# Performance work log

Hardware: AMD Instinct MI355X
Metric: run time of the kernel (lower is better)

Reference implementation:

```python
import jax, jax.numpy as jnp
import numpy as np

BETA, THR, ALPHA = 0.9, 1.0, 2.0  # snn.Leaky defaults from neuron_options + surrogate.atan(alpha=2)

# Heaviside spike with atan surrogate gradient (snntorch surrogate.atan)
@jax.custom_vjp
def spike(u):
    return (u > 0).astype(u.dtype)

def _spk_fwd(u):
    return (u > 0).astype(u.dtype), u

def _spk_bwd(u, g):
    return ((ALPHA / 2) / (1 + (jnp.pi / 2 * ALPHA * u) ** 2) * g,)

spike.defvjp(_spk_fwd, _spk_bwd)


def setup_inputs() -> dict:
    key = jax.random.key(0)
    ks = jax.random.split(key, 4)
    B, T, I, H1, H2, O = 128, 128, 1024, 2048, 2048, 512
    return {
        "x": jax.random.normal(ks[0], (B, T, I), jnp.float32),
        "W1": jax.random.normal(ks[1], (H1, I), jnp.float32) * 0.02,
        "b1": jnp.zeros((H1,), jnp.float32),
        "W2": jax.random.normal(ks[2], (H2, H1), jnp.float32) * 0.02,
        "b2": jnp.zeros((H2,), jnp.float32),
        "Wout": jax.random.normal(ks[3], (O, H2), jnp.float32) * 0.02,
        "bout": jnp.zeros((O,), jnp.float32),
    }


def _lif(v_prev, cur):
    # Module calls snn.Leaky as spike_layer(in_volt, x) -> forward(input_=v_prev, mem=cur).
    # snntorch Leaky ('subtract' reset): reset = H(mem - thr) [detached];
    # mem_new = beta*mem + input_ - reset*thr; spk = H(mem_new - thr) with atan surrogate.
    reset = jax.lax.stop_gradient((cur > THR).astype(cur.dtype))
    mem = BETA * cur + v_prev - reset * THR
    return spike(mem - THR), mem


def reference(x, W1, b1, W2, b2, Wout, bout):
    B, T, I = x.shape
    H1, H2 = W1.shape[0], W2.shape[0]
    v0 = (jnp.zeros((B, H1), x.dtype), jnp.zeros((B, H2), x.dtype))

    def step(vs, x_t):
        v1, v2 = vs
        s1, v1n = _lif(v1, x_t @ W1.T + b1)   # linear -> LIF layer 1
        s2, v2n = _lif(v2, s1 @ W2.T + b2)    # linear -> LIF layer 2
        return (v1n, v2n), s2

    _, spikes = jax.lax.scan(step, v0, jnp.swapaxes(x, 0, 1))  # spikes: (T, B, H2)
    acc = spikes.mean(0)  # 'sum' accumulator = mean over time of last-layer spikes
    return acc @ Wout.T + bout  # fc_out, identity activation
```

## Files before the change

### kernel.cpp

```cpp
#include <hip/hip_runtime.h>


typedef unsigned long long u64;
typedef __attribute__((ext_vector_type(4))) float f32x4;
typedef __attribute__((ext_vector_type(8))) short bf16x8;

__device__ __forceinline__ unsigned short f2bf(float f) {
  unsigned u = __float_as_uint(f);
  u += 0x7fff + ((u >> 16) & 1);
  return (unsigned short)(u >> 16);
}
__device__ __forceinline__ float bf2f(unsigned short h) {
  return __uint_as_float(((unsigned)h) << 16);
}
__device__ __forceinline__ void gld_lds16(const unsigned short* g, unsigned short* l) {
  __builtin_amdgcn_global_load_lds((const __attribute__((address_space(1))) void*)g,
                                   (__attribute__((address_space(3))) void*)l, 16, 0, 0);
}

__global__ void k_split4(const float4* __restrict__ src, unsigned short* __restrict__ dst,
                         int lgK, size_t total4) {
  size_t i = (size_t)blockIdx.x * 256 + threadIdx.x;
  if (i >= total4) return;
  const int K = 1 << lgK;
  size_t e = i << 2;
  size_t r = e >> lgK;
  int k = (int)(e & (size_t)(K - 1));
  float4 f = src[i];
  unsigned short h0 = f2bf(f.x), h1 = f2bf(f.y), h2 = f2bf(f.z), h3 = f2bf(f.w);
  unsigned short l0 = f2bf(f.x - bf2f(h0)), l1 = f2bf(f.y - bf2f(h1));
  unsigned short l2 = f2bf(f.z - bf2f(h2)), l3 = f2bf(f.w - bf2f(h3));
  size_t o = (r << (lgK + 1)) + (size_t)k;
  *(u64*)(dst + o)     = (u64)h0 | ((u64)h1 << 16) | ((u64)h2 << 32) | ((u64)h3 << 48);
  *(u64*)(dst + o + K) = (u64)l0 | ((u64)l1 << 16) | ((u64)l2 << 32) | ((u64)l3 << 48);
}

#define DSR4(D, BASE)                                                          \
  do {                                                                         \
    asm volatile("ds_read_b128 %0, %1" : "=v"(D[0]) : "v"(BASE));              \
    asm volatile("ds_read_b128 %0, %1 offset:2048" : "=v"(D[1]) : "v"(BASE));  \
    asm volatile("ds_read_b128 %0, %1 offset:4096" : "=v"(D[2]) : "v"(BASE));  \
    asm volatile("ds_read_b128 %0, %1 offset:6144" : "=v"(D[3]) : "v"(BASE));  \
  } while (0)
#define WAITL(N)                                                               \
  do {                                                                         \
    asm volatile("s_waitcnt lgkmcnt(" #N ")" ::: "memory");                    \
    __builtin_amdgcn_sched_barrier(0);                                         \
  } while (0)
#define VM0() asm volatile("s_waitcnt vmcnt(0)" ::: "memory")
#define BAR() __builtin_amdgcn_s_barrier()
#define MFMA16(MH, AF, BG)                                                     \
  _Pragma("unroll")                                                            \
  for (int m = 0; m < 4; ++m)                                                  \
    _Pragma("unroll")                                                          \
    for (int n = 0; n < 4; ++n)                                                \
      acc[(MH)*4 + m][n] = __builtin_amdgcn_mfma_f32_16x16x32_bf16(            \
          AF[m], BG[n], acc[(MH)*4 + m][n], 0, 0, 0);

template <int LAYER>
__global__ __launch_bounds__(512, 2)
void k_gemm_lif(const unsigned short* __restrict__ A,
                const unsigned short* __restrict__ Bw,
                const float* __restrict__ bias,
                unsigned short* __restrict__ out, int b0) {
  __shared__ __align__(128) char lds[132096];
  const int NKT = (LAYER == 1) ? 48 : 32;
  const int ldB = (LAYER == 1) ? 2048 : 4096;
  const int tid  = threadIdx.x;
  const int lane = tid & 63;
  const int w    = tid >> 6;
  const int wm = w >> 2, wn = w & 3;
  const int wr = wm * 128, wc = wn * 64;
  const int lrow = lane & 15, t4 = lane >> 4;
  const int brow = blockIdx.x * 256, bcol = blockIdx.y * 256;

  f32x4 acc[8][4];
#pragma unroll
  for (int m = 0; m < 8; ++m)
#pragma unroll
    for (int n = 0; n < 4; ++n) acc[m][n] = (f32x4){0.f, 0.f, 0.f, 0.f};

  int voffA[4], voffB[4];
  unsigned dstA[4], dstB[4];
#pragma unroll
  for (int j = 0; j < 4; ++j) {
    const int c = tid + j * 512;
    const int r = c >> 3;
    const int scol = ((c & 7) ^ (r & 7)) * 8;
    voffA[j] = (brow + r) * 2048 + scol;
    voffB[j] = (bcol + r) * ldB + scol;
    dstA[j] = (unsigned)c * 16;
    dstB[j] = 32768u + (unsigned)c * 16;
  }

  auto stage_tile = [&](int tt) {
    if (tt >= NKT) return;
    const int kb = tt * 64;
    int aoff, boff;
    if (LAYER == 1) {
      aoff = (kb < 1024) ? kb : kb - 1024;
      boff = (kb < 2048) ? kb : kb - 2048;
    } else {
      aoff = kb;
      boff = kb;
    }
    const unsigned short* Ap = A + aoff;
    const unsigned short* Bp = Bw + boff;
    char* slot = lds + (tt & 1) * 65536;
#pragma unroll
    for (int j = 0; j < 4; ++j)
      gld_lds16(Ap + voffA[j], (unsigned short*)(slot + dstA[j]));
#pragma unroll
    for (int j = 0; j < 4; ++j)
      gld_lds16(Bp + voffB[j], (unsigned short*)(slot + dstB[j]));
  };

  const unsigned ldsb = (unsigned)(size_t)(__attribute__((address_space(3))) char*)lds;
  const unsigned cA   = (unsigned)((wr + lrow) * 128);
  const unsigned cB   = (unsigned)(32768 + (wc + lrow) * 128);
  const unsigned ch0  = (unsigned)(((t4) ^ (lrow & 7)) * 16);
  const unsigned ch1  = (unsigned)(((4 + t4) ^ (lrow & 7)) * 16);

  bf16x8 afA[4], afB[4], bgA[4], bgB[4];

  stage_tile(0);
  VM0();
  BAR();
  DSR4(afA, ldsb + cA + ch0);
  DSR4(bgA, ldsb + cB + ch0);

#pragma unroll 1
  for (int t = 0; t < NKT; ++t) {
    const unsigned sA  = ldsb + (unsigned)((t & 1) * 65536);
    const unsigned sAn = ldsb + (unsigned)(((t + 1) & 1) * 65536);
    stage_tile(t + 1);
    DSR4(afB, sA + cA + 8192 + ch0);
    WAITL(4);
    __builtin_amdgcn_s_setprio(1); MFMA16(0, afA, bgA); __builtin_amdgcn_s_setprio(0);
    DSR4(afA, sA + cA + ch1);
    DSR4(bgB, sA + cB + ch1);
    WAITL(8);
    __builtin_amdgcn_s_setprio(1); MFMA16(1, afB, bgA); __builtin_amdgcn_s_setprio(0);
    DSR4(afB, sA + cA + 8192 + ch1);
    WAITL(4);
    __builtin_amdgcn_s_setprio(1); MFMA16(0, afA, bgB); __builtin_amdgcn_s_setprio(0);
    VM0();
    BAR();
    if (t + 1 < NKT) {
      DSR4(afA, sAn + cA + ch0);
      DSR4(bgA, sAn + cB + ch0);
      WAITL(8);
    } else {
      WAITL(0);
    }
    __builtin_amdgcn_s_setprio(1); MFMA16(1, afB, bgB); __builtin_amdgcn_s_setprio(0);
    BAR();
  }

  float* Ct = (float*)lds;
  const int colT  = tid & 255;
  const int batch = tid >> 8;
  const float bs = bias[bcol + colT];
  float v = 0.f;
  int cnt = 0;
  unsigned short* sp = nullptr;
  if (LAYER == 1) sp = out + (size_t)(brow + batch * 128) * 2048 + bcol + colT;
#pragma unroll
  for (int h = 0; h < 2; ++h) {
    __syncthreads();
#pragma unroll
    for (int mm = 0; mm < 4; ++mm) {
      const int m = h * 4 + mm;
#pragma unroll
      for (int n = 0; n < 4; ++n) {
        const int lr  = wm * 64 + mm * 16 + t4 * 4;
        const int col = wc + n * 16 + lrow;
#pragma unroll
        for (int r = 0; r < 4; ++r) Ct[(lr + r) * 258 + col] = acc[m][n][r];
      }
    }
    __syncthreads();
    if (LAYER == 1) {
#pragma unroll 4
      for (int tl = 0; tl < 64; ++tl) {
        const float xx = Ct[(batch * 64 + tl) * 258 + colT] + bs;
        v = 0.9f * xx + v - ((xx > 1.0f) ? 1.0f : 0.0f);
        sp[(size_t)(h * 64 + tl) * 2048] =
            (v > 1.0f) ? (unsigned short)0x3F80 : (unsigned short)0;
      }
    } else {
#pragma unroll 4
      for (int tl = 0; tl < 64; ++tl) {
        const float xx = Ct[(batch * 64 + tl) * 258 + colT] + bs;
        v = 0.9f * xx + v - ((xx > 1.0f) ? 1.0f : 0.0f);
        cnt += (v > 1.0f);
      }
    }
  }
  if (LAYER == 2)
    out[(size_t)(b0 + 2 * blockIdx.x + batch) * 2048 + bcol + colT] =
        f2bf((float)cnt * 0.0078125f);
}

__global__ void k_gemm3(const unsigned short* __restrict__ A,
                        const unsigned short* __restrict__ B,
                        float* __restrict__ C) {
  __shared__ __align__(16) unsigned short Asm[128 * 64];
  __shared__ __align__(16) unsigned short Bsm[128 * 64];
  const int tid  = threadIdx.x;
  const int bcol = blockIdx.y * 128;
  const int k0   = blockIdx.z * 256;
  const int lane = tid & 63;
  const int w    = tid >> 6;
  const int wr = (w >> 1) * 64, wc = (w & 1) * 64;
  const int lrow = lane & 15, lk = (lane >> 4) * 8;

  f32x4 acc[4][4];
#pragma unroll
  for (int m = 0; m < 4; ++m)
#pragma unroll
    for (int n = 0; n < 4; ++n) acc[m][n] = (f32x4){0.f, 0.f, 0.f, 0.f};

  for (int kt = 0; kt < 4; ++kt) {
    const int kb = k0 + kt * 64;
#pragma unroll
    for (int i = 0; i < 4; ++i) {
      int c = tid + i * 256;
      int row = c >> 3, kc = (c & 7) * 8;
      gld_lds16(A + (size_t)row * 2048 + (kb & 2047) + kc, &Asm[c * 8]);
      gld_lds16(B + (size_t)(bcol + row) * 4096 + kb + kc, &Bsm[c * 8]);
    }
    __syncthreads();
#pragma unroll
    for (int ks = 0; ks < 2; ++ks) {
      bf16x8 af[4], bg[4];
#pragma unroll
      for (int m = 0; m < 4; ++m)
        af[m] = *(const bf16x8*)&Asm[(wr + m * 16 + lrow) * 64 + ks * 32 + lk];
#pragma unroll
      for (int n = 0; n < 4; ++n)
        bg[n] = *(const bf16x8*)&Bsm[(wc + n * 16 + lrow) * 64 + ks * 32 + lk];
#pragma unroll
      for (int m = 0; m < 4; ++m)
#pragma unroll
        for (int n = 0; n < 4; ++n)
          acc[m][n] = __builtin_amdgcn_mfma_f32_16x16x32_bf16(af[m], bg[n], acc[m][n], 0, 0, 0);
    }
    __syncthreads();
  }
#pragma unroll
  for (int m = 0; m < 4; ++m)
#pragma unroll
    for (int n = 0; n < 4; ++n) {
      int r0 = wr + m * 16 + (lane >> 4) * 4;
      int c0 = bcol + wc + n * 16 + (lane & 15);
#pragma unroll
      for (int r = 0; r < 4; ++r)
        atomicAdd(&C[(size_t)(r0 + r) * 512 + c0], acc[m][n][r]);
    }
}

__global__ void k_init_out(float* __restrict__ out, const float* __restrict__ bout) {
  int i = blockIdx.x * 256 + threadIdx.x;
  out[i] = bout[i & 511];
}

extern "C" void kernel_launch(void* const* d_in, const int* in_sizes, int n_in,
                              void* d_out, int out_size, void* d_ws, size_t ws_size,
                              hipStream_t stream) {
  const float* x    = (const float*)d_in[0];
  const float* W1   = (const float*)d_in[1];
  const float* b1   = (const float*)d_in[2];
  const float* W2   = (const float*)d_in[3];
  const float* b2   = (const float*)d_in[4];
  const float* Wout = (const float*)d_in[5];
  const float* bout = (const float*)d_in[6];
  float* out = (float*)d_out;
  (void)in_sizes; (void)n_in; (void)out_size;

  char* ws = (char*)d_ws;
  size_t off = 0;
  auto alloc = [&](size_t bytes) -> void* {
    void* p = ws + off;
    off += (bytes + 255) & ~(size_t)255;
    return p;
  };
  unsigned short* W1cat = (unsigned short*)alloc((size_t)2048 * 2048 * 2);
  unsigned short* W2cat = (unsigned short*)alloc((size_t)2048 * 4096 * 2);
  unsigned short* Wocat = (unsigned short*)alloc((size_t)512 * 4096 * 2);
  unsigned short* ACC   = (unsigned short*)alloc((size_t)128 * 2048 * 2);
  const size_t fixed = off;

  int rows_c = 16384;
  while (rows_c > 1024) {
    size_t per = 2 * (((size_t)rows_c * 2048 * 2 + 255) & ~(size_t)255);
    if (fixed + per <= ws_size) break;
    rows_c >>= 1;
  }
  unsigned short* Xcat = (unsigned short*)alloc((size_t)rows_c * 2048 * 2);
  unsigned short* S1c  = (unsigned short*)alloc((size_t)rows_c * 2048 * 2);

  k_split4<<<(2048 * 256 + 255) / 256, 256, 0, stream>>>((const float4*)W1, W1cat, 10,
                                                         (size_t)2048 * 256);
  k_split4<<<(2048 * 512 + 255) / 256, 256, 0, stream>>>((const float4*)W2, W2cat, 11,
                                                         (size_t)2048 * 512);
  k_split4<<<(512 * 512 + 255) / 256, 256, 0, stream>>>((const float4*)Wout, Wocat, 11,
                                                        (size_t)512 * 512);

  const int nch = 16384 / rows_c;
  for (int c = 0; c < nch; ++c) {
    k_split4<<<rows_c, 256, 0, stream>>>((const float4*)(x + (size_t)c * rows_c * 1024),
                                         Xcat, 10, (size_t)rows_c * 256);
    k_gemm_lif<1><<<dim3(rows_c / 256, 8), 512, 0, stream>>>(Xcat, W1cat, b1, S1c, 0);
    k_gemm_lif<2><<<dim3(rows_c / 256, 8), 512, 0, stream>>>(S1c, W2cat, b2, ACC,
                                                             c * (rows_c / 128));
  }
  k_init_out<<<256, 256, 0, stream>>>(out, bout);
  k_gemm3<<<dim3(1, 4, 16), 256, 0, stream>>>(ACC, Wocat, out);
}
```

Baseline: 323.4 us.

## Load B fragments directly from global into registers and halve LDS footprint

The GEMM+LIF kernel stops staging the weight (B) tile through LDS. Each wave now loads its B fragments straight from global memory into registers, one tile ahead, and the K loop is unrolled by two to ping-pong the register buffers. LDS shrinks to A only, about 66KB, and the epilogue is restructured so only half the threads run the LIF scan over two batches in sequence, which fits the smaller LDS. The aim is to cut LDS traffic and capacity pressure, possibly allowing more blocks per CU. The cost is uncoalesced per-wave global loads of B, with B rows reloaded by each wave row, more VGPRs, and a serialized epilogue.

```diff
diff --git a/kernel.cpp b/kernel.cpp
--- a/kernel.cpp
+++ b/kernel.cpp
@@ -47,8 +47,14 @@
     asm volatile("s_waitcnt lgkmcnt(" #N ")" ::: "memory");                    \
     __builtin_amdgcn_sched_barrier(0);                                         \
   } while (0)
-#define VM0() asm volatile("s_waitcnt vmcnt(0)" ::: "memory")
+#define VMC(N)                                                                 \
+  do {                                                                         \
+    asm volatile("s_waitcnt vmcnt(" #N ")" ::: "memory");                      \
+    __builtin_amdgcn_sched_barrier(0);                                         \
+  } while (0)
 #define BAR() __builtin_amdgcn_s_barrier()
+#define SP1() __builtin_amdgcn_s_setprio(1)
+#define SP0() __builtin_amdgcn_s_setprio(0)
 #define MFMA16(MH, AF, BG)                                                     \
   _Pragma("unroll")                                                            \
   for (int m = 0; m < 4; ++m)                                                  \
@@ -57,13 +63,25 @@
       acc[(MH)*4 + m][n] = __builtin_amdgcn_mfma_f32_16x16x32_bf16(            \
           AF[m], BG[n], acc[(MH)*4 + m][n], 0, 0, 0);
 
+#define LOAD_B(TT, D, KS)                                                      \
+  do {                                                                         \
+    if ((TT) < NKT) {                                                          \
+      const int kb_ = (TT) * 64;                                               \
+      const int boff_ =                                                        \
+          (LAYER == 1) ? ((kb_ < 2048) ? kb_ : kb_ - 2048) : kb_;              \
+      _Pragma("unroll")                                                        \
+      for (int n = 0; n < 4; ++n)                                              \
+        D[n] = *(const bf16x8*)(Bw + (size_t)(browB[n] + boff_ + (KS) * 32));  \
+    }                                                                          \
+  } while (0)
+
 template <int LAYER>
 __global__ __launch_bounds__(512, 2)
 void k_gemm_lif(const unsigned short* __restrict__ A,
                 const unsigned short* __restrict__ Bw,
                 const float* __restrict__ bias,
                 unsigned short* __restrict__ out, int b0) {
-  __shared__ __align__(128) char lds[132096];
+  __shared__ __align__(128) char lds[66048];
   const int NKT = (LAYER == 1) ? 48 : 32;
   const int ldB = (LAYER == 1) ? 2048 : 4096;
   const int tid  = threadIdx.x;
@@ -80,126 +98,131 @@
 #pragma unroll
     for (int n = 0; n < 4; ++n) acc[m][n] = (f32x4){0.f, 0.f, 0.f, 0.f};
 
-  int voffA[4], voffB[4];
-  unsigned dstA[4], dstB[4];
+  int voffA[4];
+  unsigned dstA[4];
 #pragma unroll
   for (int j = 0; j < 4; ++j) {
     const int c = tid + j * 512;
     const int r = c >> 3;
     const int scol = ((c & 7) ^ (r & 7)) * 8;
     voffA[j] = (brow + r) * 2048 + scol;
-    voffB[j] = (bcol + r) * ldB + scol;
     dstA[j] = (unsigned)c * 16;
-    dstB[j] = 32768u + (unsigned)c * 16;
-  }
+  }
+  int browB[4];
+#pragma unroll
+  for (int n = 0; n < 4; ++n)
+    browB[n] = (bcol + wc + n * 16 + lrow) * ldB + t4 * 8;
 
   auto stage_tile = [&](int tt) {
     if (tt >= NKT) return;
     const int kb = tt * 64;
-    int aoff, boff;
-    if (LAYER == 1) {
-      aoff = (kb < 1024) ? kb : kb - 1024;
-      boff = (kb < 2048) ? kb : kb - 2048;
-    } else {
-      aoff = kb;
-      boff = kb;
-    }
+    const int aoff = (LAYER == 1) ? ((kb < 1024) ? kb : kb - 1024) : kb;
     const unsigned short* Ap = A + aoff;
-    const unsigned short* Bp = Bw + boff;
-    char* slot = lds + (tt & 1) * 65536;
 #pragma unroll
     for (int j = 0; j < 4; ++j)
-      gld_lds16(Ap + voffA[j], (unsigned short*)(slot + dstA[j]));
-#pragma unroll
-    for (int j = 0; j < 4; ++j)
-      gld_lds16(Bp + voffB[j], (unsigned short*)(slot + dstB[j]));
+      gld_lds16(Ap + voffA[j],
+                (unsigned short*)(lds + (tt & 1) * 32768 + dstA[j]));
   };
 
   const unsigned ldsb = (unsigned)(size_t)(__attribute__((address_space(3))) char*)lds;
-  const unsigned cA   = (unsigned)((wr + lrow) * 128);
-  const unsigned cB   = (unsigned)(32768 + (wc + lrow) * 128);
-  const unsigned ch0  = (unsigned)(((t4) ^ (lrow & 7)) * 16);
-  const unsigned ch1  = (unsigned)(((4 + t4) ^ (lrow & 7)) * 16);
-
-  bf16x8 afA[4], afB[4], bgA[4], bgB[4];
+  const unsigned cA  = (unsigned)((wr + lrow) * 128);
+  const unsigned ch0 = (unsigned)(((t4) ^ (lrow & 7)) * 16);
+  const unsigned ch1 = (unsigned)(((4 + t4) ^ (lrow & 7)) * 16);
+
+  bf16x8 afA[4], afB[4], bgE[4], bgO[4], bg1[4];
 
   stage_tile(0);
-  VM0();
+  LOAD_B(0, bgE, 0);
+  VMC(0);
   BAR();
   DSR4(afA, ldsb + cA + ch0);
-  DSR4(bgA, ldsb + cB + ch0);
+
+#define TILE_BODY(T, BGC, BGN)                                                 \
+  {                                                                            \
+    const int tt = (T);                                                        \
+    const unsigned sA  = ldsb + (unsigned)((tt & 1) * 32768);                  \
+    const unsigned sAn = ldsb + (unsigned)(((tt + 1) & 1) * 32768);            \
+    stage_tile(tt + 1);                                                        \
+    LOAD_B(tt, bg1, 1);                                \
+    LOAD_B(tt + 1, BGN, 0);                            \
+                                                                       \
+    DSR4(afB, sA + cA + 8192 + ch0);                                           \
+    WAITL(4);                                                                  \
+    SP1(); MFMA16(0, afA, BGC); SP0();                                         \
+                                                                       \
+    DSR4(afA, sA + cA + ch1);                                                  \
+    WAITL(4);                                                                  \
+    SP1(); MFMA16(1, afB, BGC); SP0();                                         \
+                                                                       \
+    DSR4(afB, sA + cA + 8192 + ch1);                                           \
+    WAITL(4);                                                                  \
+    SP1(); MFMA16(0, afA, bg1); SP0();                                         \
+    VMC(0);                          \
+    BAR();                                    \
+                                                                       \
+    if (tt + 1 < NKT) { DSR4(afA, sAn + cA + ch0); WAITL(4); }                 \
+    else              { WAITL(0); }                                            \
+    SP1(); MFMA16(1, afB, bg1); SP0();                                         \
+    BAR();                          \
+  }
 
 #pragma unroll 1
-  for (int t = 0; t < NKT; ++t) {
-    const unsigned sA  = ldsb + (unsigned)((t & 1) * 65536);
-    const unsigned sAn = ldsb + (unsigned)(((t + 1) & 1) * 65536);
-    stage_tile(t + 1);
-    DSR4(afB, sA + cA + 8192 + ch0);
-    WAITL(4);
-    __builtin_amdgcn_s_setprio(1); MFMA16(0, afA, bgA); __builtin_amdgcn_s_setprio(0);
-    DSR4(afA, sA + cA + ch1);
-    DSR4(bgB, sA + cB + ch1);
-    WAITL(8);
-    __builtin_amdgcn_s_setprio(1); MFMA16(1, afB, bgA); __builtin_amdgcn_s_setprio(0);
-    DSR4(afB, sA + cA + 8192 + ch1);
-    WAITL(4);
-    __builtin_amdgcn_s_setprio(1); MFMA16(0, afA, bgB); __builtin_amdgcn_s_setprio(0);
-    VM0();
-    BAR();
-    if (t + 1 < NKT) {
-      DSR4(afA, sAn + cA + ch0);
-      DSR4(bgA, sAn + cB + ch0);
-      WAITL(8);
-    } else {
-      WAITL(0);
-    }
-    __builtin_amdgcn_s_setprio(1); MFMA16(1, afB, bgB); __builtin_amdgcn_s_setprio(0);
-    BAR();
-  }
+  for (int t = 0; t < NKT; t += 2) {
+    TILE_BODY(t, bgE, bgO);
+    TILE_BODY(t + 1, bgO, bgE);
+  }
+#undef TILE_BODY
 
   float* Ct = (float*)lds;
-  const int colT  = tid & 255;
-  const int batch = tid >> 8;
+  const int colT = tid & 255;
   const float bs = bias[bcol + colT];
   float v = 0.f;
   int cnt = 0;
-  unsigned short* sp = nullptr;
-  if (LAYER == 1) sp = out + (size_t)(brow + batch * 128) * 2048 + bcol + colT;
-#pragma unroll
-  for (int h = 0; h < 2; ++h) {
+#pragma unroll
+  for (int q = 0; q < 4; ++q) {
+    const int b = q >> 1, h = q & 1;
     __syncthreads();
-#pragma unroll
-    for (int mm = 0; mm < 4; ++mm) {
-      const int m = h * 4 + mm;
-#pragma unroll
-      for (int n = 0; n < 4; ++n) {
-        const int lr  = wm * 64 + mm * 16 + t4 * 4;
-        const int col = wc + n * 16 + lrow;
-#pragma unroll
-        for (int r = 0; r < 4; ++r) Ct[(lr + r) * 258 + col] = acc[m][n][r];
+    if (wm == b) {
+#pragma unroll
+      for (int mm = 0; mm < 4; ++mm) {
+        const int m = h * 4 + mm;
+#pragma unroll
+        for (int n = 0; n < 4; ++n) {
+          const int lr  = mm * 16 + t4 * 4;
+          const int col = wc + n * 16 + lrow;
+#pragma unroll
+          for (int r = 0; r < 4; ++r) Ct[(lr + r) * 258 + col] = acc[m][n][r];
+        }
       }
     }
     __syncthreads();
-    if (LAYER == 1) {
+    if (tid < 256) {
+      if (LAYER == 1) {
+        unsigned short* sp =
+            out + (size_t)(brow + b * 128 + h * 64) * 2048 + bcol + colT;
 #pragma unroll 4
-      for (int tl = 0; tl < 64; ++tl) {
-        const float xx = Ct[(batch * 64 + tl) * 258 + colT] + bs;
-        v = 0.9f * xx + v - ((xx > 1.0f) ? 1.0f : 0.0f);
-        sp[(size_t)(h * 64 + tl) * 2048] =
-            (v > 1.0f) ? (unsigned short)0x3F80 : (unsigned short)0;
+        for (int tl = 0; tl < 64; ++tl) {
+          const float xx = Ct[tl * 258 + colT] + bs;
+          v = 0.9f * xx + v - ((xx > 1.0f) ? 1.0f : 0.0f);
+          sp[(size_t)tl * 2048] =
+              (v > 1.0f) ? (unsigned short)0x3F80 : (unsigned short)0;
+        }
+      } else {
+#pragma unroll 4
+        for (int tl = 0; tl < 64; ++tl) {
+          const float xx = Ct[tl * 258 + colT] + bs;
+          v = 0.9f * xx + v - ((xx > 1.0f) ? 1.0f : 0.0f);
+          cnt += (v > 1.0f);
+        }
       }
-    } else {
-#pragma unroll 4
-      for (int tl = 0; tl < 64; ++tl) {
-        const float xx = Ct[(batch * 64 + tl) * 258 + colT] + bs;
-        v = 0.9f * xx + v - ((xx > 1.0f) ? 1.0f : 0.0f);
-        cnt += (v > 1.0f);
+      if (h == 1) {
+        if (LAYER == 2)
+          out[(size_t)(b0 + 2 * blockIdx.x + b) * 2048 + bcol + colT] =
+              f2bf((float)cnt * 0.0078125f);
+        v = 0.f; cnt = 0;
       }
     }
   }
-  if (LAYER == 2)
-    out[(size_t)(b0 + 2 * blockIdx.x + batch) * 2048 + bcol + colT] =
-        f2bf((float)cnt * 0.0078125f);
 }
 
 __global__ void k_gemm3(const unsigned short* __restrict__ A,
```

New measurement: 1.033 ms. 3.19x slower.

## Shrink GEMM-LIF block tile to 256x128 with single-buffered B staging

Applied to the files above, without the earlier changes.

The fused GEMM+LIF kernels now run 256-thread blocks computing 256x128 output tiles instead of 512-thread blocks computing 256x256 tiles. LDS use drops from 132 KB to 80 KB. A stays double-buffered, while B is single-buffered and reloaded mid-iteration behind an extra barrier. The grid doubles along columns. The intent is to fit two blocks per CU and improve scheduling and tail balance, at the cost of lower operand reuse per block and an exposed wait on each B load inside the loop.

```diff
diff --git a/kernel.cpp b/kernel.cpp
--- a/kernel.cpp
+++ b/kernel.cpp
@@ -47,7 +47,11 @@
     asm volatile("s_waitcnt lgkmcnt(" #N ")" ::: "memory");                    \
     __builtin_amdgcn_sched_barrier(0);                                         \
   } while (0)
-#define VM0() asm volatile("s_waitcnt vmcnt(0)" ::: "memory")
+#define VM0()                                                                  \
+  do {                                                                         \
+    asm volatile("s_waitcnt vmcnt(0)" ::: "memory");                           \
+    __builtin_amdgcn_sched_barrier(0);                                         \
+  } while (0)
 #define BAR() __builtin_amdgcn_s_barrier()
 #define MFMA16(MH, AF, BG)                                                     \
   _Pragma("unroll")                                                            \
@@ -58,21 +62,21 @@
           AF[m], BG[n], acc[(MH)*4 + m][n], 0, 0, 0);
 
 template <int LAYER>
-__global__ __launch_bounds__(512, 2)
+__global__ __launch_bounds__(256, 2)
 void k_gemm_lif(const unsigned short* __restrict__ A,
                 const unsigned short* __restrict__ Bw,
                 const float* __restrict__ bias,
                 unsigned short* __restrict__ out, int b0) {
-  __shared__ __align__(128) char lds[132096];
+  __shared__ __align__(128) char lds[81920];
   const int NKT = (LAYER == 1) ? 48 : 32;
   const int ldB = (LAYER == 1) ? 2048 : 4096;
   const int tid  = threadIdx.x;
   const int lane = tid & 63;
   const int w    = tid >> 6;
-  const int wm = w >> 2, wn = w & 3;
+  const int wm = w >> 1, wn = w & 1;
   const int wr = wm * 128, wc = wn * 64;
   const int lrow = lane & 15, t4 = lane >> 4;
-  const int brow = blockIdx.x * 256, bcol = blockIdx.y * 256;
+  const int brow = blockIdx.x * 256, bcol = blockIdx.y * 128;
 
   f32x4 acc[8][4];
 #pragma unroll
@@ -80,50 +84,40 @@
 #pragma unroll
     for (int n = 0; n < 4; ++n) acc[m][n] = (f32x4){0.f, 0.f, 0.f, 0.f};
 
-  int voffA[4], voffB[4];
-  unsigned dstA[4], dstB[4];
-#pragma unroll
-  for (int j = 0; j < 4; ++j) {
-    const int c = tid + j * 512;
-    const int r = c >> 3;
-    const int scol = ((c & 7) ^ (r & 7)) * 8;
-    voffA[j] = (brow + r) * 2048 + scol;
-    voffB[j] = (bcol + r) * ldB + scol;
-    dstA[j] = (unsigned)c * 16;
-    dstB[j] = 32768u + (unsigned)c * 16;
-  }
-
-  auto stage_tile = [&](int tt) {
+  const int swz = ((tid & 7) ^ ((tid >> 3) & 7)) * 8;
+  const int voffA0 = (brow + (tid >> 3)) * 2048 + swz;
+  const int voffB0 = (bcol + (tid >> 3)) * ldB + swz;
+  const unsigned dst0 = (unsigned)tid * 16;
+
+  auto stage_A = [&](int tt) {
     if (tt >= NKT) return;
     const int kb = tt * 64;
-    int aoff, boff;
-    if (LAYER == 1) {
-      aoff = (kb < 1024) ? kb : kb - 1024;
-      boff = (kb < 2048) ? kb : kb - 2048;
-    } else {
-      aoff = kb;
-      boff = kb;
-    }
-    const unsigned short* Ap = A + aoff;
-    const unsigned short* Bp = Bw + boff;
-    char* slot = lds + (tt & 1) * 65536;
+    const int aoff = (LAYER == 1) ? ((kb < 1024) ? kb : kb - 1024) : kb;
+    const unsigned short* Ap = A + (aoff + voffA0);
+    char* slot = lds + (tt & 1) * 32768;
+#pragma unroll
+    for (int j = 0; j < 8; ++j)
+      gld_lds16(Ap + j * 65536, (unsigned short*)(slot + dst0 + j * 4096));
+  };
+  auto stage_B = [&](int tt) {
+    if (tt >= NKT) return;
+    const int kb = tt * 64;
+    const int boff = (LAYER == 1) ? ((kb < 2048) ? kb : kb - 2048) : kb;
+    const unsigned short* Bp = Bw + (boff + voffB0);
 #pragma unroll
     for (int j = 0; j < 4; ++j)
-      gld_lds16(Ap + voffA[j], (unsigned short*)(slot + dstA[j]));
-#pragma unroll
-    for (int j = 0; j < 4; ++j)
-      gld_lds16(Bp + voffB[j], (unsigned short*)(slot + dstB[j]));
+      gld_lds16(Bp + j * 32 * ldB, (unsigned short*)(lds + 65536 + dst0 + j * 4096));
   };
 
   const unsigned ldsb = (unsigned)(size_t)(__attribute__((address_space(3))) char*)lds;
-  const unsigned cA   = (unsigned)((wr + lrow) * 128);
-  const unsigned cB   = (unsigned)(32768 + (wc + lrow) * 128);
-  const unsigned ch0  = (unsigned)(((t4) ^ (lrow & 7)) * 16);
-  const unsigned ch1  = (unsigned)(((4 + t4) ^ (lrow & 7)) * 16);
+  const unsigned cA  = (unsigned)((wr + lrow) * 128);
+  const unsigned cB  = 65536u + (unsigned)((wc + lrow) * 128);
+  const unsigned ch0 = (unsigned)(((t4) ^ (lrow & 7)) * 16);
+  const unsigned ch1 = (unsigned)(((4 + t4) ^ (lrow & 7)) * 16);
 
   bf16x8 afA[4], afB[4], bgA[4], bgB[4];
 
-  stage_tile(0);
+  stage_A(0); stage_B(0);
   VM0();
   BAR();
   DSR4(afA, ldsb + cA + ch0);
@@ -131,35 +125,35 @@
 
 #pragma unroll 1
   for (int t = 0; t < NKT; ++t) {
-    const unsigned sA  = ldsb + (unsigned)((t & 1) * 65536);
-    const unsigned sAn = ldsb + (unsigned)(((t + 1) & 1) * 65536);
-    stage_tile(t + 1);
+    const unsigned sA  = ldsb + (unsigned)((t & 1) * 32768);
+    const unsigned sAn = ldsb + (unsigned)(((t + 1) & 1) * 32768);
+    stage_A(t + 1);
     DSR4(afB, sA + cA + 8192 + ch0);
     WAITL(4);
     __builtin_amdgcn_s_setprio(1); MFMA16(0, afA, bgA); __builtin_amdgcn_s_setprio(0);
     DSR4(afA, sA + cA + ch1);
-    DSR4(bgB, sA + cB + ch1);
+    DSR4(bgB, ldsb + cB + ch1);
     WAITL(8);
     __builtin_amdgcn_s_setprio(1); MFMA16(1, afB, bgA); __builtin_amdgcn_s_setprio(0);
     DSR4(afB, sA + cA + 8192 + ch1);
     WAITL(4);
     __builtin_amdgcn_s_setprio(1); MFMA16(0, afA, bgB); __builtin_amdgcn_s_setprio(0);
+    BAR();
+    stage_B(t + 1);
+    WAITL(0);
     VM0();
     BAR();
     if (t + 1 < NKT) {
       DSR4(afA, sAn + cA + ch0);
-      DSR4(bgA, sAn + cB + ch0);
-      WAITL(8);
-    } else {
-      WAITL(0);
+      DSR4(bgA, ldsb + cB + ch0);
     }
     __builtin_amdgcn_s_setprio(1); MFMA16(1, afB, bgB); __builtin_amdgcn_s_setprio(0);
     BAR();
   }
 
   float* Ct = (float*)lds;
-  const int colT  = tid & 255;
-  const int batch = tid >> 8;
+  const int colT  = tid & 127;
+  const int batch = tid >> 7;
   const float bs = bias[bcol + colT];
   float v = 0.f;
   int cnt = 0;
@@ -176,14 +170,14 @@
         const int lr  = wm * 64 + mm * 16 + t4 * 4;
         const int col = wc + n * 16 + lrow;
 #pragma unroll
-        for (int r = 0; r < 4; ++r) Ct[(lr + r) * 258 + col] = acc[m][n][r];
+        for (int r = 0; r < 4; ++r) Ct[(lr + r) * 130 + col] = acc[m][n][r];
       }
     }
     __syncthreads();
     if (LAYER == 1) {
 #pragma unroll 4
       for (int tl = 0; tl < 64; ++tl) {
-        const float xx = Ct[(batch * 64 + tl) * 258 + colT] + bs;
+        const float xx = Ct[(batch * 64 + tl) * 130 + colT] + bs;
         v = 0.9f * xx + v - ((xx > 1.0f) ? 1.0f : 0.0f);
         sp[(size_t)(h * 64 + tl) * 2048] =
             (v > 1.0f) ? (unsigned short)0x3F80 : (unsigned short)0;
@@ -191,7 +185,7 @@
     } else {
 #pragma unroll 4
       for (int tl = 0; tl < 64; ++tl) {
-        const float xx = Ct[(batch * 64 + tl) * 258 + colT] + bs;
+        const float xx = Ct[(batch * 64 + tl) * 130 + colT] + bs;
         v = 0.9f * xx + v - ((xx > 1.0f) ? 1.0f : 0.0f);
         cnt += (v > 1.0f);
       }
@@ -311,9 +305,9 @@
   for (int c = 0; c < nch; ++c) {
     k_split4<<<rows_c, 256, 0, stream>>>((const float4*)(x + (size_t)c * rows_c * 1024),
                                          Xcat, 10, (size_t)rows_c * 256);
-    k_gemm_lif<1><<<dim3(rows_c / 256, 8), 512, 0, stream>>>(Xcat, W1cat, b1, S1c, 0);
-    k_gemm_lif<2><<<dim3(rows_c / 256, 8), 512, 0, stream>>>(S1c, W2cat, b2, ACC,
-                                                             c * (rows_c / 128));
+    k_gemm_lif<1><<<dim3(rows_c / 256, 16), 256, 0, stream>>>(Xcat, W1cat, b1, S1c, 0);
+    k_gemm_lif<2><<<dim3(rows_c / 256, 16), 256, 0, stream>>>(S1c, W2cat, b2, ACC,
+                                                              c * (rows_c / 128));
   }
   k_init_out<<<256, 256, 0, stream>>>(out, bout);
   k_gemm3<<<dim3(1, 4, 16), 256, 0, stream>>>(ACC, Wocat, out);
```

Measured after the change: 346.2 us. +7.0%, slower.

## Quantize W2 to int8 and run layer-2 GEMM with int8 MFMA

Applied to the files above, without the earlier changes.

Replaces the split bf16 hi/lo representation of W2 with per-row int8 quantization and a float scale. Layer-1 spikes are stored as bytes, and layer 2 uses i32 16x16x64 int8 MFMA with a triple-buffered LDS pipeline. This halves the effective K and the spike-buffer traffic and uses the higher int8 matrix throughput. The trade-off is that W2 precision drops to 8 bits, which may flip spikes near threshold.

```diff
diff --git a/kernel.cpp b/kernel.cpp
--- a/kernel.cpp
+++ b/kernel.cpp
@@ -4,6 +4,7 @@
 typedef unsigned long long u64;
 typedef __attribute__((ext_vector_type(4))) float f32x4;
 typedef __attribute__((ext_vector_type(8))) short bf16x8;
+typedef __attribute__((ext_vector_type(4))) int i32x4;
 
 __device__ __forceinline__ unsigned short f2bf(float f) {
   unsigned u = __float_as_uint(f);
@@ -13,7 +14,7 @@
 __device__ __forceinline__ float bf2f(unsigned short h) {
   return __uint_as_float(((unsigned)h) << 16);
 }
-__device__ __forceinline__ void gld_lds16(const unsigned short* g, unsigned short* l) {
+__device__ __forceinline__ void gld_lds16(const void* g, void* l) {
   __builtin_amdgcn_global_load_lds((const __attribute__((address_space(1))) void*)g,
                                    (__attribute__((address_space(3))) void*)l, 16, 0, 0);
 }
@@ -35,6 +36,32 @@
   *(u64*)(dst + o + K) = (u64)l0 | ((u64)l1 << 16) | ((u64)l2 << 32) | ((u64)l3 << 48);
 }
 
+__global__ void k_quant_w2(const float* __restrict__ W2, signed char* __restrict__ W2q,
+                           float* __restrict__ scl) {
+  __shared__ float red[4];
+  const int r = blockIdx.x;
+  const int tid = threadIdx.x;
+  const float* row = W2 + (size_t)r * 2048;
+  float vbuf[8];
+  float mx = 0.f;
+#pragma unroll
+  for (int k = 0; k < 8; ++k) {
+    vbuf[k] = row[tid + k * 256];
+    mx = fmaxf(mx, fabsf(vbuf[k]));
+  }
+#pragma unroll
+  for (int o = 32; o; o >>= 1) mx = fmaxf(mx, __shfl_xor(mx, o));
+  if ((tid & 63) == 0) red[tid >> 6] = mx;
+  __syncthreads();
+  mx = fmaxf(fmaxf(red[0], red[1]), fmaxf(red[2], red[3]));
+  mx = fmaxf(mx, 1e-20f);
+  const float inv = 127.f / mx;
+  if (tid == 0) scl[r] = mx * (1.f / 127.f);
+#pragma unroll
+  for (int k = 0; k < 8; ++k)
+    W2q[(size_t)r * 2048 + tid + k * 256] = (signed char)__float2int_rn(vbuf[k] * inv);
+}
+
 #define DSR4(D, BASE)                                                          \
   do {                                                                         \
     asm volatile("ds_read_b128 %0, %1" : "=v"(D[0]) : "v"(BASE));              \
@@ -42,13 +69,26 @@
     asm volatile("ds_read_b128 %0, %1 offset:4096" : "=v"(D[2]) : "v"(BASE));  \
     asm volatile("ds_read_b128 %0, %1 offset:6144" : "=v"(D[3]) : "v"(BASE));  \
   } while (0)
+#define DSR4_I8(D, BASE)                                                       \
+  do {                                                                         \
+    asm volatile("ds_read_b128 %0, %1" : "=v"(D[0]) : "v"(BASE));              \
+    asm volatile("ds_read_b128 %0, %1 offset:1024" : "=v"(D[1]) : "v"(BASE));  \
+    asm volatile("ds_read_b128 %0, %1 offset:2048" : "=v"(D[2]) : "v"(BASE));  \
+    asm volatile("ds_read_b128 %0, %1 offset:3072" : "=v"(D[3]) : "v"(BASE));  \
+  } while (0)
 #define WAITL(N)                                                               \
   do {                                                                         \
     asm volatile("s_waitcnt lgkmcnt(" #N ")" ::: "memory");                    \
     __builtin_amdgcn_sched_barrier(0);                                         \
   } while (0)
-#define VM0() asm volatile("s_waitcnt vmcnt(0)" ::: "memory")
+#define VMC(N)                                                                 \
+  do {                                                                         \
+    asm volatile("s_waitcnt vmcnt(" #N ")" ::: "memory");                      \
+    __builtin_amdgcn_sched_barrier(0);                                         \
+  } while (0)
 #define BAR() __builtin_amdgcn_s_barrier()
+#define SP1() __builtin_amdgcn_s_setprio(1)
+#define SP0() __builtin_amdgcn_s_setprio(0)
 #define MFMA16(MH, AF, BG)                                                     \
   _Pragma("unroll")                                                            \
   for (int m = 0; m < 4; ++m)                                                  \
@@ -56,16 +96,21 @@
     for (int n = 0; n < 4; ++n)                                                \
       acc[(MH)*4 + m][n] = __builtin_amdgcn_mfma_f32_16x16x32_bf16(            \
           AF[m], BG[n], acc[(MH)*4 + m][n], 0, 0, 0);
-
-template <int LAYER>
+#define MFMA16_I8(MH, AF, BG)                                                  \
+  _Pragma("unroll")                                                            \
+  for (int m = 0; m < 4; ++m)                                                  \
+    _Pragma("unroll")                                                          \
+    for (int n = 0; n < 4; ++n)                                                \
+      acc[(MH)*4 + m][n] = __builtin_amdgcn_mfma_i32_16x16x64_i8(              \
+          AF[m], BG[n], acc[(MH)*4 + m][n], 0, 0, 0);
+
 __global__ __launch_bounds__(512, 2)
-void k_gemm_lif(const unsigned short* __restrict__ A,
-                const unsigned short* __restrict__ Bw,
-                const float* __restrict__ bias,
-                unsigned short* __restrict__ out, int b0) {
+void k_gemm1_lif(const unsigned short* __restrict__ A,
+                 const unsigned short* __restrict__ Bw,
+                 const float* __restrict__ bias,
+                 unsigned char* __restrict__ out) {
   __shared__ __align__(128) char lds[132096];
-  const int NKT = (LAYER == 1) ? 48 : 32;
-  const int ldB = (LAYER == 1) ? 2048 : 4096;
+  const int NKT = 48;
   const int tid  = threadIdx.x;
   const int lane = tid & 63;
   const int w    = tid >> 6;
@@ -88,31 +133,24 @@
     const int r = c >> 3;
     const int scol = ((c & 7) ^ (r & 7)) * 8;
     voffA[j] = (brow + r) * 2048 + scol;
-    voffB[j] = (bcol + r) * ldB + scol;
+    voffB[j] = (bcol + r) * 2048 + scol;
     dstA[j] = (unsigned)c * 16;
     dstB[j] = 32768u + (unsigned)c * 16;
   }
-
   auto stage_tile = [&](int tt) {
     if (tt >= NKT) return;
     const int kb = tt * 64;
-    int aoff, boff;
-    if (LAYER == 1) {
-      aoff = (kb < 1024) ? kb : kb - 1024;
-      boff = (kb < 2048) ? kb : kb - 2048;
-    } else {
-      aoff = kb;
-      boff = kb;
-    }
+    const int aoff = (kb < 1024) ? kb : kb - 1024;
+    const int boff = (kb < 2048) ? kb : kb - 2048;
     const unsigned short* Ap = A + aoff;
     const unsigned short* Bp = Bw + boff;
     char* slot = lds + (tt & 1) * 65536;
 #pragma unroll
     for (int j = 0; j < 4; ++j)
-      gld_lds16(Ap + voffA[j], (unsigned short*)(slot + dstA[j]));
+      gld_lds16(Ap + voffA[j], slot + dstA[j]);
 #pragma unroll
     for (int j = 0; j < 4; ++j)
-      gld_lds16(Bp + voffB[j], (unsigned short*)(slot + dstB[j]));
+      gld_lds16(Bp + voffB[j], slot + dstB[j]);
   };
 
   const unsigned ldsb = (unsigned)(size_t)(__attribute__((address_space(3))) char*)lds;
@@ -124,7 +162,7 @@
   bf16x8 afA[4], afB[4], bgA[4], bgB[4];
 
   stage_tile(0);
-  VM0();
+  asm volatile("s_waitcnt vmcnt(0)" ::: "memory");
   BAR();
   DSR4(afA, ldsb + cA + ch0);
   DSR4(bgA, ldsb + cB + ch0);
@@ -136,15 +174,15 @@
     stage_tile(t + 1);
     DSR4(afB, sA + cA + 8192 + ch0);
     WAITL(4);
-    __builtin_amdgcn_s_setprio(1); MFMA16(0, afA, bgA); __builtin_amdgcn_s_setprio(0);
+    SP1(); MFMA16(0, afA, bgA); SP0();
     DSR4(afA, sA + cA + ch1);
     DSR4(bgB, sA + cB + ch1);
     WAITL(8);
-    __builtin_amdgcn_s_setprio(1); MFMA16(1, afB, bgA); __builtin_amdgcn_s_setprio(0);
+    SP1(); MFMA16(1, afB, bgA); SP0();
     DSR4(afB, sA + cA + 8192 + ch1);
     WAITL(4);
-    __builtin_amdgcn_s_setprio(1); MFMA16(0, afA, bgB); __builtin_amdgcn_s_setprio(0);
-    VM0();
+    SP1(); MFMA16(0, afA, bgB); SP0();
+    asm volatile("s_waitcnt vmcnt(0)" ::: "memory");
     BAR();
     if (t + 1 < NKT) {
       DSR4(afA, sAn + cA + ch0);
@@ -153,7 +191,7 @@
     } else {
       WAITL(0);
     }
-    __builtin_amdgcn_s_setprio(1); MFMA16(1, afB, bgB); __builtin_amdgcn_s_setprio(0);
+    SP1(); MFMA16(1, afB, bgB); SP0();
     BAR();
   }
 
@@ -162,9 +200,7 @@
   const int batch = tid >> 8;
   const float bs = bias[bcol + colT];
   float v = 0.f;
-  int cnt = 0;
-  unsigned short* sp = nullptr;
-  if (LAYER == 1) sp = out + (size_t)(brow + batch * 128) * 2048 + bcol + colT;
+  unsigned char* sp = out + (size_t)(brow + batch * 128) * 2048 + bcol + colT;
 #pragma unroll
   for (int h = 0; h < 2; ++h) {
     __syncthreads();
@@ -180,26 +216,134 @@
       }
     }
     __syncthreads();
-    if (LAYER == 1) {
 #pragma unroll 4
-      for (int tl = 0; tl < 64; ++tl) {
-        const float xx = Ct[(batch * 64 + tl) * 258 + colT] + bs;
-        v = 0.9f * xx + v - ((xx > 1.0f) ? 1.0f : 0.0f);
-        sp[(size_t)(h * 64 + tl) * 2048] =
-            (v > 1.0f) ? (unsigned short)0x3F80 : (unsigned short)0;
+    for (int tl = 0; tl < 64; ++tl) {
+      const float xx = Ct[(batch * 64 + tl) * 258 + colT] + bs;
+      v = 0.9f * xx + v - ((xx > 1.0f) ? 1.0f : 0.0f);
+      sp[(size_t)(h * 64 + tl) * 2048] = (v > 1.0f) ? 1 : 0;
+    }
+  }
+}
+
+__global__ __launch_bounds__(512, 2)
+void k_gemm2_lif_i8(const signed char* __restrict__ A,
+                    const signed char* __restrict__ Bq,
+                    const float* __restrict__ scl,
+                    const float* __restrict__ bias,
+                    unsigned short* __restrict__ out, int b0) {
+  __shared__ __align__(128) char lds[132096];
+  const int NKT = 32;
+  const int tid  = threadIdx.x;
+  const int lane = tid & 63;
+  const int w    = tid >> 6;
+  const int wm = w >> 2, wn = w & 3;
+  const int wr = wm * 128, wc = wn * 64;
+  const int lrow = lane & 15, t4 = lane >> 4;
+  const int brow = blockIdx.x * 256, bcol = blockIdx.y * 256;
+
+  i32x4 acc[8][4];
+#pragma unroll
+  for (int m = 0; m < 8; ++m)
+#pragma unroll
+    for (int n = 0; n < 4; ++n) acc[m][n] = (i32x4){0, 0, 0, 0};
+
+  int voffA[2], voffB[2];
+  unsigned dstA[2], dstB[2];
+#pragma unroll
+  for (int j = 0; j < 2; ++j) {
+    const int c = tid + j * 512;
+    const int r = c >> 2;
+    const int sc = ((c & 3) ^ ((r >> 1) & 3)) * 16;
+    voffA[j] = (brow + r) * 2048 + sc;
+    voffB[j] = (bcol + r) * 2048 + sc;
+    dstA[j] = (unsigned)c * 16;
+    dstB[j] = 16384u + (unsigned)c * 16;
+  }
+  auto stage_tile = [&](int tt) {
+    if (tt >= NKT) return;
+    const int kb = tt * 64;
+    char* slot = lds + (tt % 3) * 32768;
+#pragma unroll
+    for (int j = 0; j < 2; ++j)
+      gld_lds16(A + kb + voffA[j], slot + dstA[j]);
+#pragma unroll
+    for (int j = 0; j < 2; ++j)
+      gld_lds16(Bq + kb + voffB[j], slot + dstB[j]);
+  };
+
+  const unsigned ldsb = (unsigned)(size_t)(__attribute__((address_space(3))) char*)lds;
+  const unsigned cA  = (unsigned)((wr + lrow) * 64);
+  const unsigned cB  = 16384u + (unsigned)((wc + lrow) * 64);
+  const unsigned chi = (unsigned)((t4 ^ ((lrow >> 1) & 3)) * 16);
+
+  i32x4 afA[4], afB[4], bgA[4], bgB[4];
+
+  stage_tile(0); stage_tile(1);
+  VMC(4);
+  BAR();
+  DSR4_I8(afA, ldsb + cA + chi);
+  DSR4_I8(bgA, ldsb + cB + chi);
+
+#define TILE_I8(T, BGC, BGN)                                                   \
+  {                                                                            \
+    const int tt = (T);                                                        \
+    const unsigned s  = ldsb + (unsigned)((tt % 3) * 32768);                   \
+    const unsigned sn = ldsb + (unsigned)(((tt + 1) % 3) * 32768);             \
+    stage_tile(tt + 2);                                                        \
+    if (tt + 2 < NKT) { VMC(4); } else { VMC(0); }       \
+    BAR();                                                                     \
+    DSR4_I8(afB, s + cA + 4096 + chi);                                         \
+    WAITL(4);                                                                  \
+    SP1(); MFMA16_I8(0, afA, BGC); SP0();                                      \
+    if (tt + 1 < NKT) {                                                        \
+      DSR4_I8(afA, sn + cA + chi);                                             \
+      DSR4_I8(BGN, sn + cB + chi);                                             \
+      WAITL(8);                                                                \
+    } else {                                                                   \
+      WAITL(0);                                                                \
+    }                                                                          \
+    SP1(); MFMA16_I8(1, afB, BGC); SP0();                                      \
+    BAR();                                                                     \
+  }
+
+#pragma unroll 1
+  for (int t = 0; t < NKT; t += 2) {
+    TILE_I8(t, bgA, bgB);
+    TILE_I8(t + 1, bgB, bgA);
+  }
+#undef TILE_I8
+
+  int* Cti = (int*)lds;
+  const int colT  = tid & 255;
+  const int batch = tid >> 8;
+  const float bs = bias[bcol + colT];
+  const float sc = scl[bcol + colT];
+  float v = 0.f;
+  int cnt = 0;
+#pragma unroll
+  for (int h = 0; h < 2; ++h) {
+    __syncthreads();
+#pragma unroll
+    for (int mm = 0; mm < 4; ++mm) {
+      const int m = h * 4 + mm;
+#pragma unroll
+      for (int n = 0; n < 4; ++n) {
+        const int lr  = wm * 64 + mm * 16 + t4 * 4;
+        const int col = wc + n * 16 + lrow;
+#pragma unroll
+        for (int r = 0; r < 4; ++r) Cti[(lr + r) * 258 + col] = acc[m][n][r];
       }
-    } else {
+    }
+    __syncthreads();
 #pragma unroll 4
-      for (int tl = 0; tl < 64; ++tl) {
-        const float xx = Ct[(batch * 64 + tl) * 258 + colT] + bs;
-        v = 0.9f * xx + v - ((xx > 1.0f) ? 1.0f : 0.0f);
-        cnt += (v > 1.0f);
-      }
-    }
-  }
-  if (LAYER == 2)
-    out[(size_t)(b0 + 2 * blockIdx.x + batch) * 2048 + bcol + colT] =
-        f2bf((float)cnt * 0.0078125f);
+    for (int tl = 0; tl < 64; ++tl) {
+      const float xx = (float)Cti[(batch * 64 + tl) * 258 + colT] * sc + bs;
+      v = 0.9f * xx + v - ((xx > 1.0f) ? 1.0f : 0.0f);
+      cnt += (v > 1.0f);
+    }
+  }
+  out[(size_t)(b0 + 2 * blockIdx.x + batch) * 2048 + bcol + colT] =
+      f2bf((float)cnt * 0.0078125f);
 }
 
 __global__ void k_gemm3(const unsigned short* __restrict__ A,
@@ -286,24 +430,25 @@
     return p;
   };
   unsigned short* W1cat = (unsigned short*)alloc((size_t)2048 * 2048 * 2);
-  unsigned short* W2cat = (unsigned short*)alloc((size_t)2048 * 4096 * 2);
+  signed char*    W2q   = (signed char*)alloc((size_t)2048 * 2048);
+  float*          scl   = (float*)alloc((size_t)2048 * 4);
   unsigned short* Wocat = (unsigned short*)alloc((size_t)512 * 4096 * 2);
   unsigned short* ACC   = (unsigned short*)alloc((size_t)128 * 2048 * 2);
   const size_t fixed = off;
 
   int rows_c = 16384;
   while (rows_c > 1024) {
-    size_t per = 2 * (((size_t)rows_c * 2048 * 2 + 255) & ~(size_t)255);
+    size_t per = (((size_t)rows_c * 2048 * 2 + 255) & ~(size_t)255) +
+                 (((size_t)rows_c * 2048 + 255) & ~(size_t)255);
     if (fixed + per <= ws_size) break;
     rows_c >>= 1;
   }
   unsigned short* Xcat = (unsigned short*)alloc((size_t)rows_c * 2048 * 2);
-  unsigned short* S1c  = (unsigned short*)alloc((size_t)rows_c * 2048 * 2);
+  unsigned char*  S1c  = (unsigned char*)alloc((size_t)rows_c * 2048);
 
   k_split4<<<(2048 * 256 + 255) / 256, 256, 0, stream>>>((const float4*)W1, W1cat, 10,
                                                          (size_t)2048 * 256);
-  k_split4<<<(2048 * 512 + 255) / 256, 256, 0, stream>>>((const float4*)W2, W2cat, 11,
-                                                         (size_t)2048 * 512);
+  k_quant_w2<<<2048, 256, 0, stream>>>(W2, W2q, scl);
   k_split4<<<(512 * 512 + 255) / 256, 256, 0, stream>>>((const float4*)Wout, Wocat, 11,
                                                         (size_t)512 * 512);
 
@@ -311,9 +456,9 @@
   for (int c = 0; c < nch; ++c) {
     k_split4<<<rows_c, 256, 0, stream>>>((const float4*)(x + (size_t)c * rows_c * 1024),
                                          Xcat, 10, (size_t)rows_c * 256);
-    k_gemm_lif<1><<<dim3(rows_c / 256, 8), 512, 0, stream>>>(Xcat, W1cat, b1, S1c, 0);
-    k_gemm_lif<2><<<dim3(rows_c / 256, 8), 512, 0, stream>>>(S1c, W2cat, b2, ACC,
-                                                             c * (rows_c / 128));
+    k_gemm1_lif<<<dim3(rows_c / 256, 8), 512, 0, stream>>>(Xcat, W1cat, b1, S1c);
+    k_gemm2_lif_i8<<<dim3(rows_c / 256, 8), 512, 0, stream>>>(
+        (const signed char*)S1c, W2q, scl, b2, ACC, c * (rows_c / 128));
   }
   k_init_out<<<256, 256, 0, stream>>>(out, bout);
   k_gemm3<<<dim3(1, 4, 16), 256, 0, stream>>>(ACC, Wocat, out);
```

Result: faster. 283.9 us (-12.2%).
